# Performance work log

Measured on AMD Instinct MI355X. Metric: run time of the kernel, lower is better.

The kernel has to match this reference:

```python
import jax, jax.numpy as jnp
import numpy as np

N = 2_097_152
EPS = 1e-6


def _tri(x):
    # triangleWave (period 2), maps R -> [0, 1]; applied to 'normalize=True' tables
    return 2.0 * jnp.abs(x / 2.0 - jnp.floor(x / 2.0 + 0.5))


def _grid2d(uv, table, bilinear, normalize):
    # uv: (N,2) in [0,1); table: (U,V,L)
    t = _tri(table) if normalize else table
    U, V, _ = t.shape
    u = jnp.clip(uv[:, 0], 0.0, 1.0 - EPS) * (U - 1)
    v = jnp.clip(uv[:, 1], 0.0, 1.0 - EPS) * (V - 1)
    if bilinear:
        u0 = jnp.floor(u)
        v0 = jnp.floor(v)
        fu = (u - u0)[:, None]
        fv = (v - v0)[:, None]
        u0i = u0.astype(jnp.int32)
        v0i = v0.astype(jnp.int32)
        u1i = jnp.minimum(u0i + 1, U - 1)
        v1i = jnp.minimum(v0i + 1, V - 1)
        return (t[u0i, v0i] * (1 - fu) * (1 - fv)
                + t[u1i, v0i] * fu * (1 - fv)
                + t[u0i, v1i] * (1 - fu) * fv
                + t[u1i, v1i] * fu * fv)
    return t[jnp.round(u).astype(jnp.int32), jnp.round(v).astype(jnp.int32)]


def _grid1d(u, table, bilinear, normalize):
    # u: (N,) in [0,1); table: (U,L)
    t = _tri(table) if normalize else table
    U, _ = t.shape
    uu = jnp.clip(u, 0.0, 1.0 - EPS) * (U - 1)
    if bilinear:
        u0 = jnp.floor(uu)
        fu = (uu - u0)[:, None]
        u0i = u0.astype(jnp.int32)
        u1i = jnp.minimum(u0i + 1, U - 1)
        return t[u0i] * (1 - fu) + t[u1i] * fu
    return t[jnp.round(uu).astype(jnp.int32)]


def setup_inputs() -> dict:
    key = jax.random.key(0)
    ks = jax.random.split(key, 17)
    mk = lambda i, shape: jax.random.uniform(ks[i], shape, dtype=jnp.float32)
    names = ["roughNoh", "anisoToh", "nDotLV", "tDotLV", "metalLoh",
             "subCg", "spst", "shst", "lumCs"]
    d = {n: mk(i, (N, 2)) for i, n in enumerate(names)}
    d["tabRAEnc"] = mk(9, (2048, 2048, 2))
    d["tabCgEnc"] = mk(10, (2048, 1))
    d["tabRSEnc"] = mk(11, (64, 64, 3))
    d["tabRADec"] = mk(12, (48, 48, 3))
    d["tabCgDec"] = mk(13, (96, 2))
    d["tabLVR"] = mk(14, (32, 32, 1))
    d["tabLV"] = mk(15, (32, 32, 4))
    d["tabNHL"] = mk(16, (32, 32, 4))
    return d


def reference(roughNoh, anisoToh, nDotLV, tDotLV, metalLoh, subCg, spst, shst,
              lumCs, tabRAEnc, tabCgEnc, tabRSEnc, tabRADec, tabCgDec,
              tabLVR, tabLV, tabNHL):
    raIn = jnp.stack((roughNoh[:, 0], anisoToh[:, 0]), axis=1)  # (N,2)
    metallicity = metalLoh[:, 0]
    # ---- encoder: LUT lookups + elementwise mixing coefficients ----
    ra = _grid2d(raIn, tabRAEnc, bilinear=False, normalize=True)           # (N,2)
    cg = _grid1d(subCg[:, 1], tabCgEnc, bilinear=False, normalize=True)    # (N,1)
    rsEnc = _grid2d(jnp.concatenate((raIn[:, 0:1], subCg[:, 0:1]), axis=1),
                    tabRSEnc, bilinear=True, normalize=True)               # (N,3)
    cd = (1 - metallicity) * lumCs[:, 0]
    cm0 = (spst[:, 0] * 0.1 * (1 - metallicity) * spst[:, 1]
           + metallicity * lumCs[:, 0])[:, None]
    cm1 = (spst[:, 0] * 0.1 * (1 - metallicity) * (1 - spst[:, 1]))[:, None]
    cs0 = (shst[:, 0] * (1 - metallicity) * shst[:, 1])[:, None]
    cs1 = (shst[:, 0] * (1 - metallicity) * (1 - shst[:, 1]))[:, None]
    cc = (0.25 * 0.25 * lumCs[:, 1])[:, None]
    rsCd = rsEnc * cd[:, None]                                             # (N,3)
    # ---- decoder LUTs ----
    raCoefs = _grid2d(ra, tabRADec, bilinear=True, normalize=False)        # (N,3)
    cgCoefs = _grid1d(cg[:, 0], tabCgDec, bilinear=True, normalize=False)  # (N,2)
    vTerm = _grid2d(jnp.concatenate((nDotLV[:, 0:1] * nDotLV[:, 1:2],
                                     ra[:, 0:1]), axis=1),
                    tabLVR, bilinear=True, normalize=True)                 # (N,1)
    nlvCoefs = _grid2d(nDotLV, tabLV, bilinear=True, normalize=True)       # (N,4)
    nhlCoefs = _grid2d(jnp.stack((metalLoh[:, 1], nDotLV[:, 0]), axis=1),
                       tabNHL, bilinear=True, normalize=True)              # (N,4)
    # ---- elementwise shading combination ----
    noh2 = roughNoh[:, 1] ** 2
    den = raCoefs[:, 0] * anisoToh[:, 1] ** 2 + raCoefs[:, 1] * noh2 + raCoefs[:, 2]
    dTerm = (0.25 / (nDotLV[:, 1] * den ** 2))[:, None]
    x = (rsCd[:, 0:1] * metalLoh[:, 1:2] * nlvCoefs[:, 1:2]
         + rsCd[:, 1:2] * nlvCoefs[:, 2:3]
         + rsCd[:, 2:3] * nlvCoefs[:, 3:4]
         + cm0 * vTerm * nhlCoefs[:, 2:3] * dTerm
         + cs0 * nhlCoefs[:, 0:1])
    y = (((1 - cm1) * nhlCoefs[:, 3:4] + cm1) * vTerm * dTerm
         + cs1 * nhlCoefs[:, 0:1]
         + cc * nhlCoefs[:, 1:2] * nlvCoefs[:, 0:1]
           / (nDotLV[:, 1] * (cgCoefs[:, 0] * noh2 + cgCoefs[:, 1]))[:, None])
    return jnp.concatenate((x, y), axis=1)  # (N,2)
```

## Files before the change

### kernel.cpp

```cpp
#include <hip/hip_runtime.h>
#include <hip/hip_fp16.h>

#define CLIP_HI (1.0f - 1e-6f)

typedef float f4v __attribute__((ext_vector_type(4)));

__device__ __forceinline__ float tri_(float x) {
    return 2.0f * fabsf(x * 0.5f - floorf(x * 0.5f + 0.5f));
}

__device__ __forceinline__ float clamp01(float x) {
    return fminf(fmaxf(x, 0.0f), CLIP_HI);
}

__device__ __forceinline__ float4 nt_load4(const float* p) {
    f4v v = __builtin_nontemporal_load((const f4v*)p);
    return make_float4(v.x, v.y, v.z, v.w);
}
__device__ __forceinline__ void nt_store4(float* p, float4 v) {
    f4v t = {v.x, v.y, v.z, v.w};
    __builtin_nontemporal_store(t, (f4v*)p);
}

struct H4 { __half2 xy, zw; };

struct BW {
    int i00, i10, i01, i11;
    float w00, w10, w01, w11;
};

template <int U, int V>
__device__ __forceinline__ BW bw2d(float uc, float vc) {
    float u = clamp01(uc) * (float)(U - 1);
    float v = clamp01(vc) * (float)(V - 1);
    float u0f = floorf(u), v0f = floorf(v);
    float fu = u - u0f, fv = v - v0f;
    int u0 = (int)u0f, v0 = (int)v0f;
    int u1 = min(u0 + 1, U - 1);
    int v1 = min(v0 + 1, V - 1);
    BW r;
    r.i00 = u0 * V + v0;
    r.i10 = u1 * V + v0;
    r.i01 = u0 * V + v1;
    r.i11 = u1 * V + v1;
    float gu = 1.0f - fu, gv = 1.0f - fv;
    r.w00 = gu * gv; r.w10 = fu * gv; r.w01 = gu * fv; r.w11 = fu * fv;
    return r;
}

__device__ __forceinline__ float4 h4_blend(H4 A, H4 B, H4 C, H4 D, const BW& b) {
    float2 Axy = __half22float2(A.xy), Azw = __half22float2(A.zw);
    float2 Bxy = __half22float2(B.xy), Bzw = __half22float2(B.zw);
    float2 Cxy = __half22float2(C.xy), Czw = __half22float2(C.zw);
    float2 Dxy = __half22float2(D.xy), Dzw = __half22float2(D.zw);
    return make_float4(
        Axy.x * b.w00 + Bxy.x * b.w10 + Cxy.x * b.w01 + Dxy.x * b.w11,
        Axy.y * b.w00 + Bxy.y * b.w10 + Cxy.y * b.w01 + Dxy.y * b.w11,
        Azw.x * b.w00 + Bzw.x * b.w10 + Czw.x * b.w01 + Dzw.x * b.w11,
        Azw.y * b.w00 + Bzw.y * b.w10 + Czw.y * b.w01 + Dzw.y * b.w11);
}

__global__ __launch_bounds__(256) void prep_kernel(const float* __restrict__ t_rs,
                                                   const float* __restrict__ t_cge,
                                                   const float* __restrict__ t_cgd,
                                                   H4* __restrict__ o_rs,
                                                   float2* __restrict__ o_cg) {
    int j = blockIdx.x * 256 + threadIdx.x;
    if (j < 64 * 64) {
        float a = tri_(t_rs[j * 3 + 0]);
        float b = tri_(t_rs[j * 3 + 1]);
        float c = tri_(t_rs[j * 3 + 2]);
        H4 h;
        h.xy = __floats2half2_rn(a, b);
        h.zw = __floats2half2_rn(c, 0.0f);
        o_rs[j] = h;
    }
    int c = j - 64 * 64;
    if (c >= 0 && c < 2048) {
        float cg = tri_(t_cge[c]);
        float u = clamp01(cg) * 95.0f;
        float u0f = floorf(u);
        float fu = u - u0f;
        int u0 = (int)u0f;
        int u1 = min(u0 + 1, 95);
        float2 a = ((const float2*)t_cgd)[u0];
        float2 b = ((const float2*)t_cgd)[u1];
        o_cg[c] = make_float2(a.x * (1.0f - fu) + b.x * fu,
                              a.y * (1.0f - fu) + b.y * fu);
    }
}

__device__ __forceinline__ float2 gatherRA(const float* __restrict__ tabRAEnc,
                                           float rNx, float aTx) {
    int ui = (int)rintf(clamp01(rNx) * 2047.0f);
    int vi = (int)rintf(clamp01(aTx) * 2047.0f);
    return ((const float2*)tabRAEnc)[ui * 2048 + vi];
}

template <bool USE_WS>
__device__ __forceinline__ float2 shadeB(
    float rNx, float rNy, float aTy, float nLVx, float nLVy,
    float mLx, float mLy, float sCx, float sCy, float spx, float spy,
    float shx, float shy, float lCx, float lCy,
    float2 raT,
    const float* __restrict__ tabRSEnc, const H4* __restrict__ rsPacked,
    const float* __restrict__ tabCgEnc, const float* __restrict__ tabCgDec,
    const float2* __restrict__ cgComp,
    const H4* sRADec, const __half* sLVR,
    const H4* sLV, const H4* sNHL)
{
    float rs0, rs1, rs2;
    {
        BW b = bw2d<64, 64>(rNx, sCx);
        if constexpr (USE_WS) {
            float4 r = h4_blend(rsPacked[b.i00], rsPacked[b.i10],
                                rsPacked[b.i01], rsPacked[b.i11], b);
            rs0 = r.x; rs1 = r.y; rs2 = r.z;
        } else {
            const float* p00 = tabRSEnc + b.i00 * 3;
            const float* p10 = tabRSEnc + b.i10 * 3;
            const float* p01 = tabRSEnc + b.i01 * 3;
            const float* p11 = tabRSEnc + b.i11 * 3;
            rs0 = tri_(p00[0]) * b.w00 + tri_(p10[0]) * b.w10 + tri_(p01[0]) * b.w01 + tri_(p11[0]) * b.w11;
            rs1 = tri_(p00[1]) * b.w00 + tri_(p10[1]) * b.w10 + tri_(p01[1]) * b.w01 + tri_(p11[1]) * b.w11;
            rs2 = tri_(p00[2]) * b.w00 + tri_(p10[2]) * b.w10 + tri_(p01[2]) * b.w01 + tri_(p11[2]) * b.w11;
        }
    }

    float2 cgC;
    {
        int ci = (int)rintf(clamp01(sCy) * 2047.0f);
        if constexpr (USE_WS) {
            cgC = cgComp[ci];
        } else {
            float cg = tri_(tabCgEnc[ci]);
            float u = clamp01(cg) * 95.0f;
            float u0f = floorf(u);
            float fu = u - u0f;
            int u0 = (int)u0f;
            int u1 = min(u0 + 1, 95);
            float2 a = ((const float2*)tabCgDec)[u0];
            float2 b = ((const float2*)tabCgDec)[u1];
            cgC = make_float2(a.x * (1.0f - fu) + b.x * fu,
                              a.y * (1.0f - fu) + b.y * fu);
        }
    }

    float4 nlv, nhl;
    {
        BW b = bw2d<32, 32>(nLVx, nLVy);
        nlv = h4_blend(sLV[b.i00], sLV[b.i10], sLV[b.i01], sLV[b.i11], b);
    }
    {
        BW b = bw2d<32, 32>(mLy, nLVx);
        nhl = h4_blend(sNHL[b.i00], sNHL[b.i10], sNHL[b.i01], sNHL[b.i11], b);
    }

    float ra0 = tri_(raT.x);
    float ra1 = tri_(raT.y);

    float raC0, raC1, raC2;
    {
        BW b = bw2d<48, 48>(ra0, ra1);
        float4 r = h4_blend(sRADec[b.i00], sRADec[b.i10],
                            sRADec[b.i01], sRADec[b.i11], b);
        raC0 = r.x; raC1 = r.y; raC2 = r.z;
    }

    float vTerm;
    {
        BW b = bw2d<32, 32>(nLVx * nLVy, ra0);
        vTerm = __half2float(sLVR[b.i00]) * b.w00 + __half2float(sLVR[b.i10]) * b.w10 +
                __half2float(sLVR[b.i01]) * b.w01 + __half2float(sLVR[b.i11]) * b.w11;
    }

    float met = mLx;
    float om  = 1.0f - met;
    float cd  = om * lCx;
    float cm0 = spx * 0.1f * om * spy + met * lCx;
    float cm1 = spx * 0.1f * om * (1.0f - spy);
    float cs0 = shx * om * shy;
    float cs1 = shx * om * (1.0f - shy);
    float cc  = 0.0625f * lCy;

    float noh2 = rNy * rNy;
    float den  = raC0 * aTy * aTy + raC1 * noh2 + raC2;
    float dTerm = 0.25f / (nLVy * den * den);

    float x = rs0 * cd * mLy * nlv.y + rs1 * cd * nlv.z + rs2 * cd * nlv.w
            + cm0 * vTerm * nhl.z * dTerm + cs0 * nhl.x;

    float y = ((1.0f - cm1) * nhl.w + cm1) * vTerm * dTerm
            + cs1 * nhl.x
            + cc * nhl.y * nlv.x / (nLVy * (cgC.x * noh2 + cgC.y));

    return make_float2(x, y);
}

template <bool USE_WS>
__global__ __launch_bounds__(512, 6) void disney_main(
    const float* __restrict__ roughNoh,
    const float* __restrict__ anisoToh,
    const float* __restrict__ nDotLV,
    const float* __restrict__ metalLoh,
    const float* __restrict__ subCg,
    const float* __restrict__ spst,
    const float* __restrict__ shst,
    const float* __restrict__ lumCs,
    const float* __restrict__ tabRAEnc,
    const float* __restrict__ tabCgEnc,
    const float* __restrict__ tabCgDec,
    const float* __restrict__ tabRSEnc,
    const H4*    __restrict__ rsPacked,
    const float2* __restrict__ cgComp,
    const float* __restrict__ tabRADec,
    const float* __restrict__ tabLVR,
    const float* __restrict__ tabLV,
    const float* __restrict__ tabNHL,
    float* __restrict__ out,
    int n)
{
    __shared__ H4      sRADec[48 * 48];
    __shared__ __half  sLVR[1024];
    __shared__ H4      sLV[1024];
    __shared__ H4      sNHL[1024];

    int tid = threadIdx.x;

    for (int j = tid; j < 48 * 48; j += 512) {
        H4 h;
        h.xy = __floats2half2_rn(tabRADec[j * 3 + 0], tabRADec[j * 3 + 1]);
        h.zw = __floats2half2_rn(tabRADec[j * 3 + 2], 0.0f);
        sRADec[j] = h;
    }
#pragma unroll
    for (int k = 0; k < 2; ++k) {
        int j = tid + k * 512;
        sLVR[j] = __float2half(tri_(tabLVR[j]));
        float4 v = ((const float4*)tabLV)[j];
        H4 h; h.xy = __floats2half2_rn(tri_(v.x), tri_(v.y));
              h.zw = __floats2half2_rn(tri_(v.z), tri_(v.w));
        sLV[j] = h;
        float4 w = ((const float4*)tabNHL)[j];
        H4 h2; h2.xy = __floats2half2_rn(tri_(w.x), tri_(w.y));
               h2.zw = __floats2half2_rn(tri_(w.z), tri_(w.w));
        sNHL[j] = h2;
    }
    __syncthreads();

    int P = (n + 1) >> 1;
    int H = (P + 1) >> 1;
    int t = blockIdx.x * 512 + tid;
    if (t >= H) return;
    int p1 = t;
    int p2 = t + H;

    bool full1 = (2 * p1 + 1) < n;
    bool full2 = (p2 < P) && ((2 * p2 + 1) < n);

    if (full1 && full2) {
        float4 rN1 = nt_load4(roughNoh + 4 * p1);
        float4 aT1 = nt_load4(anisoToh + 4 * p1);
        float4 rN2 = nt_load4(roughNoh + 4 * p2);
        float4 aT2 = nt_load4(anisoToh + 4 * p2);

        float2 raT0 = gatherRA(tabRAEnc, rN1.x, aT1.x);
        float2 raT1 = gatherRA(tabRAEnc, rN1.z, aT1.z);
        float2 raT2 = gatherRA(tabRAEnc, rN2.x, aT2.x);
        float2 raT3 = gatherRA(tabRAEnc, rN2.z, aT2.z);

        float4 nLV1 = nt_load4(nDotLV   + 4 * p1);
        float4 mL1  = nt_load4(metalLoh + 4 * p1);
        float4 sC1  = nt_load4(subCg    + 4 * p1);
        float4 sp1  = nt_load4(spst     + 4 * p1);
        float4 sh1  = nt_load4(shst     + 4 * p1);
        float4 lC1  = nt_load4(lumCs    + 4 * p1);
        float4 nLV2 = nt_load4(nDotLV   + 4 * p2);
        float4 mL2  = nt_load4(metalLoh + 4 * p2);
        float4 sC2  = nt_load4(subCg    + 4 * p2);
        float4 sp2  = nt_load4(spst     + 4 * p2);
        float4 sh2  = nt_load4(shst     + 4 * p2);
        float4 lC2  = nt_load4(lumCs    + 4 * p2);

        float2 r0 = shadeB<USE_WS>(rN1.x, rN1.y, aT1.y, nLV1.x, nLV1.y,
                                   mL1.x, mL1.y, sC1.x, sC1.y, sp1.x, sp1.y,
                                   sh1.x, sh1.y, lC1.x, lC1.y, raT0,
                                   tabRSEnc, rsPacked, tabCgEnc, tabCgDec, cgComp,
                                   sRADec, sLVR, sLV, sNHL);
        float2 r1 = shadeB<USE_WS>(rN1.z, rN1.w, aT1.w, nLV1.z, nLV1.w,
                                   mL1.z, mL1.w, sC1.z, sC1.w, sp1.z, sp1.w,
                                   sh1.z, sh1.w, lC1.z, lC1.w, raT1,
                                   tabRSEnc, rsPacked, tabCgEnc, tabCgDec, cgComp,
                                   sRADec, sLVR, sLV, sNHL);
        nt_store4(out + 4 * p1, make_float4(r0.x, r0.y, r1.x, r1.y));

        float2 r2 = shadeB<USE_WS>(rN2.x, rN2.y, aT2.y, nLV2.x, nLV2.y,
                                   mL2.x, mL2.y, sC2.x, sC2.y, sp2.x, sp2.y,
                                   sh2.x, sh2.y, lC2.x, lC2.y, raT2,
                                   tabRSEnc, rsPacked, tabCgEnc, tabCgDec, cgComp,
                                   sRADec, sLVR, sLV, sNHL);
        float2 r3 = shadeB<USE_WS>(rN2.z, rN2.w, aT2.w, nLV2.z, nLV2.w,
                                   mL2.z, mL2.w, sC2.z, sC2.w, sp2.z, sp2.w,
                                   sh2.z, sh2.w, lC2.z, lC2.w, raT3,
                                   tabRSEnc, rsPacked, tabCgEnc, tabCgDec, cgComp,
                                   sRADec, sLVR, sLV, sNHL);
        nt_store4(out + 4 * p2, make_float4(r2.x, r2.y, r3.x, r3.y));
    } else {
        int es[4] = { 2 * p1, 2 * p1 + 1,
                      (p2 < P) ? 2 * p2 : n, (p2 < P) ? 2 * p2 + 1 : n };
#pragma unroll
        for (int k = 0; k < 4; ++k) {
            int e = es[k];
            if (e >= n) continue;
            float2 rN  = ((const float2*)roughNoh)[e];
            float2 aT  = ((const float2*)anisoToh)[e];
            float2 nLV = ((const float2*)nDotLV)[e];
            float2 mL  = ((const float2*)metalLoh)[e];
            float2 sC  = ((const float2*)subCg)[e];
            float2 sp  = ((const float2*)spst)[e];
            float2 sh  = ((const float2*)shst)[e];
            float2 lC  = ((const float2*)lumCs)[e];
            float2 raT = gatherRA(tabRAEnc, rN.x, aT.x);
            float2 r = shadeB<USE_WS>(rN.x, rN.y, aT.y, nLV.x, nLV.y,
                                      mL.x, mL.y, sC.x, sC.y, sp.x, sp.y,
                                      sh.x, sh.y, lC.x, lC.y, raT,
                                      tabRSEnc, rsPacked, tabCgEnc, tabCgDec, cgComp,
                                      sRADec, sLVR, sLV, sNHL);
            ((float2*)out)[e] = r;
        }
    }
}

extern "C" void kernel_launch(void* const* d_in, const int* in_sizes, int n_in,
                              void* d_out, int out_size, void* d_ws, size_t ws_size,
                              hipStream_t stream) {
    const float* roughNoh = (const float*)d_in[0];
    const float* anisoToh = (const float*)d_in[1];
    const float* nDotLV   = (const float*)d_in[2];
    const float* metalLoh = (const float*)d_in[4];
    const float* subCg    = (const float*)d_in[5];
    const float* spst     = (const float*)d_in[6];
    const float* shst     = (const float*)d_in[7];
    const float* lumCs    = (const float*)d_in[8];
    const float* tabRAEnc = (const float*)d_in[9];
    const float* tabCgEnc = (const float*)d_in[10];
    const float* tabRSEnc = (const float*)d_in[11];
    const float* tabRADec = (const float*)d_in[12];
    const float* tabCgDec = (const float*)d_in[13];
    const float* tabLVR   = (const float*)d_in[14];
    const float* tabLV    = (const float*)d_in[15];
    const float* tabNHL   = (const float*)d_in[16];

    int n = in_sizes[0] / 2;
    float* out = (float*)d_out;

    const int block = 512;
    int P = (n + 1) / 2;
    int H = (P + 1) / 2;
    int grid = (H + block - 1) / block;

    const size_t WS_NEED = 64 * 64 * sizeof(H4) + 2048 * sizeof(float2);
    bool use_ws = ws_size >= WS_NEED;
    H4*     ws_rs = (H4*)d_ws;
    float2* ws_cg = (float2*)((char*)d_ws + 64 * 64 * sizeof(H4));

    if (use_ws) {
        const int prep_items = 64 * 64 + 2048;
        prep_kernel<<<(prep_items + 255) / 256, 256, 0, stream>>>(
            tabRSEnc, tabCgEnc, tabCgDec, ws_rs, ws_cg);
        disney_main<true><<<grid, block, 0, stream>>>(
            roughNoh, anisoToh, nDotLV, metalLoh, subCg, spst, shst, lumCs,
            tabRAEnc, tabCgEnc, tabCgDec, tabRSEnc, ws_rs, ws_cg,
            tabRADec, tabLVR, tabLV, tabNHL, out, n);
    } else {
        disney_main<false><<<grid, block, 0, stream>>>(
            roughNoh, anisoToh, nDotLV, metalLoh, subCg, spst, shst, lumCs,
            tabRAEnc, tabCgEnc, tabCgDec, tabRSEnc, ws_rs, ws_cg,
            tabRADec, tabLVR, tabLV, tabNHL, out, n);
    }
}
```

Before: 244.0 us.

## Move RADec table to global workspace, shrink blocks, halve cg precision

The kernel no longer builds the 48x48 RADec decode table in shared memory inside every block. A prep kernel now writes it once to the workspace as packed halves, and the main kernel gathers it from global memory through the cache. Block size drops from 512 to 256 with new launch bounds, which cuts per-block shared memory, and the Cg composite table is stored as half2. Bilinear neighbour indices are computed by adding offsets instead of clamping, relying on the input clamp to keep the upper neighbour in range. The trade-off is cached global gathers in place of LDS reads, plus somewhat lower precision on the Cg coefficients.

Result: no change. 244.9 us (+0.4%).

```diff
diff --git a/kernel.cpp b/kernel.cpp
--- a/kernel.cpp
+++ b/kernel.cpp
@@ -36,13 +36,11 @@
     float u0f = floorf(u), v0f = floorf(v);
     float fu = u - u0f, fv = v - v0f;
     int u0 = (int)u0f, v0 = (int)v0f;
-    int u1 = min(u0 + 1, U - 1);
-    int v1 = min(v0 + 1, V - 1);
     BW r;
     r.i00 = u0 * V + v0;
-    r.i10 = u1 * V + v0;
-    r.i01 = u0 * V + v1;
-    r.i11 = u1 * V + v1;
+    r.i10 = r.i00 + V;
+    r.i01 = r.i00 + 1;
+    r.i11 = r.i10 + 1;
     float gu = 1.0f - fu, gv = 1.0f - fv;
     r.w00 = gu * gv; r.w10 = fu * gv; r.w01 = gu * fv; r.w11 = fu * fv;
     return r;
@@ -63,8 +61,10 @@
 __global__ __launch_bounds__(256) void prep_kernel(const float* __restrict__ t_rs,
                                                    const float* __restrict__ t_cge,
                                                    const float* __restrict__ t_cgd,
+                                                   const float* __restrict__ t_rad,
                                                    H4* __restrict__ o_rs,
-                                                   float2* __restrict__ o_cg) {
+                                                   __half2* __restrict__ o_cg,
+                                                   H4* __restrict__ o_rad) {
     int j = blockIdx.x * 256 + threadIdx.x;
     if (j < 64 * 64) {
         float a = tri_(t_rs[j * 3 + 0]);
@@ -75,9 +75,8 @@
         h.zw = __floats2half2_rn(c, 0.0f);
         o_rs[j] = h;
     }
-    int c = j - 64 * 64;
-    if (c >= 0 && c < 2048) {
-        float cg = tri_(t_cge[c]);
+    if (j < 2048) {
+        float cg = tri_(t_cge[j]);
         float u = clamp01(cg) * 95.0f;
         float u0f = floorf(u);
         float fu = u - u0f;
@@ -85,8 +84,14 @@
         int u1 = min(u0 + 1, 95);
         float2 a = ((const float2*)t_cgd)[u0];
         float2 b = ((const float2*)t_cgd)[u1];
-        o_cg[c] = make_float2(a.x * (1.0f - fu) + b.x * fu,
-                              a.y * (1.0f - fu) + b.y * fu);
+        o_cg[j] = __floats2half2_rn(a.x * (1.0f - fu) + b.x * fu,
+                                    a.y * (1.0f - fu) + b.y * fu);
+    }
+    if (j < 48 * 48) {
+        H4 h;
+        h.xy = __floats2half2_rn(t_rad[j * 3 + 0], t_rad[j * 3 + 1]);
+        h.zw = __floats2half2_rn(t_rad[j * 3 + 2], 0.0f);
+        o_rad[j] = h;
     }
 }
 
@@ -104,10 +109,10 @@
     float shx, float shy, float lCx, float lCy,
     float2 raT,
     const float* __restrict__ tabRSEnc, const H4* __restrict__ rsPacked,
+    const float* __restrict__ tabRADec, const H4* __restrict__ raDec,
     const float* __restrict__ tabCgEnc, const float* __restrict__ tabCgDec,
-    const float2* __restrict__ cgComp,
-    const H4* sRADec, const __half* sLVR,
-    const H4* sLV, const H4* sNHL)
+    const __half2* __restrict__ cgComp,
+    const __half* sLVR, const H4* sLV, const H4* sNHL)
 {
     float rs0, rs1, rs2;
     {
@@ -131,7 +136,7 @@
     {
         int ci = (int)rintf(clamp01(sCy) * 2047.0f);
         if constexpr (USE_WS) {
-            cgC = cgComp[ci];
+            cgC = __half22float2(cgComp[ci]);
         } else {
             float cg = tri_(tabCgEnc[ci]);
             float u = clamp01(cg) * 95.0f;
@@ -162,9 +167,19 @@
     float raC0, raC1, raC2;
     {
         BW b = bw2d<48, 48>(ra0, ra1);
-        float4 r = h4_blend(sRADec[b.i00], sRADec[b.i10],
-                            sRADec[b.i01], sRADec[b.i11], b);
-        raC0 = r.x; raC1 = r.y; raC2 = r.z;
+        if constexpr (USE_WS) {
+            float4 r = h4_blend(raDec[b.i00], raDec[b.i10],
+                                raDec[b.i01], raDec[b.i11], b);
+            raC0 = r.x; raC1 = r.y; raC2 = r.z;
+        } else {
+            const float* p00 = tabRADec + b.i00 * 3;
+            const float* p10 = tabRADec + b.i10 * 3;
+            const float* p01 = tabRADec + b.i01 * 3;
+            const float* p11 = tabRADec + b.i11 * 3;
+            raC0 = p00[0] * b.w00 + p10[0] * b.w10 + p01[0] * b.w01 + p11[0] * b.w11;
+            raC1 = p00[1] * b.w00 + p10[1] * b.w10 + p01[1] * b.w01 + p11[1] * b.w11;
+            raC2 = p00[2] * b.w00 + p10[2] * b.w10 + p01[2] * b.w01 + p11[2] * b.w11;
+        }
     }
 
     float vTerm;
@@ -198,7 +213,7 @@
 }
 
 template <bool USE_WS>
-__global__ __launch_bounds__(512, 6) void disney_main(
+__global__ __launch_bounds__(256, 4) void disney_main(
     const float* __restrict__ roughNoh,
     const float* __restrict__ anisoToh,
     const float* __restrict__ nDotLV,
@@ -211,31 +226,25 @@
     const float* __restrict__ tabCgEnc,
     const float* __restrict__ tabCgDec,
     const float* __restrict__ tabRSEnc,
+    const float* __restrict__ tabRADec,
     const H4*    __restrict__ rsPacked,
-    const float2* __restrict__ cgComp,
-    const float* __restrict__ tabRADec,
+    const __half2* __restrict__ cgComp,
+    const H4*    __restrict__ raDec,
     const float* __restrict__ tabLVR,
     const float* __restrict__ tabLV,
     const float* __restrict__ tabNHL,
     float* __restrict__ out,
     int n)
 {
-    __shared__ H4      sRADec[48 * 48];
     __shared__ __half  sLVR[1024];
     __shared__ H4      sLV[1024];
     __shared__ H4      sNHL[1024];
 
     int tid = threadIdx.x;
 
-    for (int j = tid; j < 48 * 48; j += 512) {
-        H4 h;
-        h.xy = __floats2half2_rn(tabRADec[j * 3 + 0], tabRADec[j * 3 + 1]);
-        h.zw = __floats2half2_rn(tabRADec[j * 3 + 2], 0.0f);
-        sRADec[j] = h;
-    }
 #pragma unroll
-    for (int k = 0; k < 2; ++k) {
-        int j = tid + k * 512;
+    for (int k = 0; k < 4; ++k) {
+        int j = tid + k * 256;
         sLVR[j] = __float2half(tri_(tabLVR[j]));
         float4 v = ((const float4*)tabLV)[j];
         H4 h; h.xy = __floats2half2_rn(tri_(v.x), tri_(v.y));
@@ -250,7 +259,7 @@
 
     int P = (n + 1) >> 1;
     int H = (P + 1) >> 1;
-    int t = blockIdx.x * 512 + tid;
+    int t = blockIdx.x * 256 + tid;
     if (t >= H) return;
     int p1 = t;
     int p2 = t + H;
@@ -285,25 +294,29 @@
         float2 r0 = shadeB<USE_WS>(rN1.x, rN1.y, aT1.y, nLV1.x, nLV1.y,
                                    mL1.x, mL1.y, sC1.x, sC1.y, sp1.x, sp1.y,
                                    sh1.x, sh1.y, lC1.x, lC1.y, raT0,
-                                   tabRSEnc, rsPacked, tabCgEnc, tabCgDec, cgComp,
-                                   sRADec, sLVR, sLV, sNHL);
+                                   tabRSEnc, rsPacked, tabRADec, raDec,
+                                   tabCgEnc, tabCgDec, cgComp,
+                                   sLVR, sLV, sNHL);
         float2 r1 = shadeB<USE_WS>(rN1.z, rN1.w, aT1.w, nLV1.z, nLV1.w,
                                    mL1.z, mL1.w, sC1.z, sC1.w, sp1.z, sp1.w,
                                    sh1.z, sh1.w, lC1.z, lC1.w, raT1,
-                                   tabRSEnc, rsPacked, tabCgEnc, tabCgDec, cgComp,
-                                   sRADec, sLVR, sLV, sNHL);
+                                   tabRSEnc, rsPacked, tabRADec, raDec,
+                                   tabCgEnc, tabCgDec, cgComp,
+                                   sLVR, sLV, sNHL);
         nt_store4(out + 4 * p1, make_float4(r0.x, r0.y, r1.x, r1.y));
 
         float2 r2 = shadeB<USE_WS>(rN2.x, rN2.y, aT2.y, nLV2.x, nLV2.y,
                                    mL2.x, mL2.y, sC2.x, sC2.y, sp2.x, sp2.y,
                                    sh2.x, sh2.y, lC2.x, lC2.y, raT2,
-                                   tabRSEnc, rsPacked, tabCgEnc, tabCgDec, cgComp,
-                                   sRADec, sLVR, sLV, sNHL);
+                                   tabRSEnc, rsPacked, tabRADec, raDec,
+                                   tabCgEnc, tabCgDec, cgComp,
+                                   sLVR, sLV, sNHL);
         float2 r3 = shadeB<USE_WS>(rN2.z, rN2.w, aT2.w, nLV2.z, nLV2.w,
                                    mL2.z, mL2.w, sC2.z, sC2.w, sp2.z, sp2.w,
                                    sh2.z, sh2.w, lC2.z, lC2.w, raT3,
-                                   tabRSEnc, rsPacked, tabCgEnc, tabCgDec, cgComp,
-                                   sRADec, sLVR, sLV, sNHL);
+                                   tabRSEnc, rsPacked, tabRADec, raDec,
+                                   tabCgEnc, tabCgDec, cgComp,
+                                   sLVR, sLV, sNHL);
         nt_store4(out + 4 * p2, make_float4(r2.x, r2.y, r3.x, r3.y));
     } else {
         int es[4] = { 2 * p1, 2 * p1 + 1,
@@ -324,8 +337,9 @@
             float2 r = shadeB<USE_WS>(rN.x, rN.y, aT.y, nLV.x, nLV.y,
                                       mL.x, mL.y, sC.x, sC.y, sp.x, sp.y,
                                       sh.x, sh.y, lC.x, lC.y, raT,
-                                      tabRSEnc, rsPacked, tabCgEnc, tabCgDec, cgComp,
-                                      sRADec, sLVR, sLV, sNHL);
+                                      tabRSEnc, rsPacked, tabRADec, raDec,
+                                      tabCgEnc, tabCgDec, cgComp,
+                                      sLVR, sLV, sNHL);
             ((float2*)out)[e] = r;
         }
     }
@@ -354,28 +368,32 @@
     int n = in_sizes[0] / 2;
     float* out = (float*)d_out;
 
-    const int block = 512;
+    const int block = 256;
     int P = (n + 1) / 2;
     int H = (P + 1) / 2;
     int grid = (H + block - 1) / block;
 
-    const size_t WS_NEED = 64 * 64 * sizeof(H4) + 2048 * sizeof(float2);
+    const size_t OFF_CG  = 64 * 64 * sizeof(H4);
+    const size_t OFF_RAD = OFF_CG + 2048 * sizeof(__half2);
+    const size_t WS_NEED = OFF_RAD + 48 * 48 * sizeof(H4);
     bool use_ws = ws_size >= WS_NEED;
-    H4*     ws_rs = (H4*)d_ws;
-    float2* ws_cg = (float2*)((char*)d_ws + 64 * 64 * sizeof(H4));
+    H4*      ws_rs  = (H4*)d_ws;
+    __half2* ws_cg  = (__half2*)((char*)d_ws + OFF_CG);
+    H4*      ws_rad = (H4*)((char*)d_ws + OFF_RAD);
 
     if (use_ws) {
-        const int prep_items = 64 * 64 + 2048;
-        prep_kernel<<<(prep_items + 255) / 256, 256, 0, stream>>>(
-            tabRSEnc, tabCgEnc, tabCgDec, ws_rs, ws_cg);
+        prep_kernel<<<(64 * 64 + 255) / 256, 256, 0, stream>>>(
+            tabRSEnc, tabCgEnc, tabCgDec, tabRADec, ws_rs, ws_cg, ws_rad);
         disney_main<true><<<grid, block, 0, stream>>>(
             roughNoh, anisoToh, nDotLV, metalLoh, subCg, spst, shst, lumCs,
-            tabRAEnc, tabCgEnc, tabCgDec, tabRSEnc, ws_rs, ws_cg,
-            tabRADec, tabLVR, tabLV, tabNHL, out, n);
+            tabRAEnc, tabCgEnc, tabCgDec, tabRSEnc, tabRADec,
+            ws_rs, ws_cg, ws_rad,
+            tabLVR, tabLV, tabNHL, out, n);
     } else {
         disney_main<false><<<grid, block, 0, stream>>>(
             roughNoh, anisoToh, nDotLV, metalLoh, subCg, spst, shst, lumCs,
-            tabRAEnc, tabCgEnc, tabCgDec, tabRSEnc, ws_rs, ws_cg,
-            tabRADec, tabLVR, tabLV, tabNHL, out, n);
-    }
-}
+            tabRAEnc, tabCgEnc, tabCgDec, tabRSEnc, tabRADec,
+            ws_rs, ws_cg, ws_rad,
+            tabLVR, tabLV, tabNHL, out, n);
+    }
+}
```
